# Optimization experiments

Hardware: AMD Instinct MI355X
Metric: run time of the kernel (lower is better)

## Reference

```python
import jax, jax.numpy as jnp
import numpy as np

B, H, K = 4096, 256, 16
INPUT_DIM, XPRIME_DIM = 8, 64
D = INPUT_DIM * XPRIME_DIM  # 512
LN_EPS = 1e-5


def setup_inputs() -> dict:
    key = jax.random.key(0)
    ks = jax.random.split(key, 12)
    s1 = 1.0  # Linear(1, D): fan_in=1
    sD = 1.0 / np.sqrt(D)
    sH = 1.0 / np.sqrt(H)
    return {
        "h_prev_rnn": jax.random.normal(ks[0], (B, H), jnp.float32),
        "x_l": jax.random.normal(ks[1], (B, INPUT_DIM), jnp.float32),
        "x_ext": jax.random.normal(ks[2], (B, K), jnp.float32),
        # stacked per-expert MetaNet params
        "meta_w1": jax.random.uniform(ks[3], (K, D), jnp.float32, -s1, s1),
        "meta_b1": jax.random.uniform(ks[4], (K, D), jnp.float32, -s1, s1),
        "meta_w2": jax.random.uniform(ks[5], (K, D, D), jnp.float32, -sD, sD),
        "meta_b2": jax.random.uniform(ks[6], (K, D), jnp.float32, -sD, sD),
        # gating net
        "gw1": jax.random.uniform(ks[7], (H, H), jnp.float32, -sH, sH),
        "gb1": jax.random.uniform(ks[8], (H,), jnp.float32, -sH, sH),
        "gw2": jax.random.uniform(ks[9], (H, K), jnp.float32, -sH, sH),
        "gb2": jax.random.uniform(ks[10], (K,), jnp.float32, -sH, sH),
        # LayerNorm([input_dim, xprime_dim]) affine params
        "ln_g": jnp.ones((INPUT_DIM, XPRIME_DIM), jnp.float32),
        "ln_b": jnp.zeros((INPUT_DIM, XPRIME_DIM), jnp.float32),
        "theta0": jnp.zeros((1, INPUT_DIM, XPRIME_DIM), jnp.float32),
    }


def reference(h_prev_rnn, x_l, x_ext, meta_w1, meta_b1, meta_w2, meta_b2,
              gw1, gb1, gw2, gb2, ln_g, ln_b, theta0):
    # MetaNet layer1 (Linear(1, D)): scalar input per expert -> [B, K, D]
    h1 = jnp.tanh(x_ext[:, :, None] * meta_w1[None] + meta_b1[None])
    # MetaNet layer2: per-expert DxD GEMM
    h2 = jnp.tanh(jnp.einsum('bkd,kde->bke', h1, meta_w2) + meta_b2[None])
    W = h2.reshape(h2.shape[0], K, INPUT_DIM, XPRIME_DIM)  # [B,K,i,e]
    # LayerNorm over last two dims jointly, affine
    mu = W.mean(axis=(-2, -1), keepdims=True)
    var = W.var(axis=(-2, -1), keepdims=True)
    W = (W - mu) * jax.lax.rsqrt(var + LN_EPS) * ln_g + ln_b
    # gating: softmax over experts (epoch/top_k = None path)
    logits = jnp.tanh(h_prev_rnn @ gw1 + gb1) @ gw2 + gb2
    gates = jax.nn.softmax(logits, axis=-1)  # [B, K]
    theta = jnp.einsum('bk,bkie->bie', gates, W) + theta0  # [B, i, e]
    x_prime = jnp.einsum('bi,bie->be', x_l, theta)  # [B, e]
    return (x_prime, theta)
```

## Files before the change

kernel.cpp:

```cpp
#include <hip/hip_runtime.h>
#include <stdint.h>

#define NB 4096
#define NH 256
#define NK 16
#define ND 512
#define NC 48
#define NM 48
#define RCHEB 7.0f
#define PI_F 3.14159265358979323846f
#define CCPART (NK * 2 * ND * 32)

typedef _Float16 f16;
using half8   = __attribute__((ext_vector_type(8))) _Float16;
using float4v = __attribute__((ext_vector_type(4))) float;

__device__ __forceinline__ float fast_tanh(float x) {
  float e = __builtin_amdgcn_exp2f(x * 2.88539008177793f);
  return 1.0f - 2.0f * __builtin_amdgcn_rcpf(e + 1.0f);
}

template <int CTRL>
__device__ __forceinline__ float dpp_addstep(float x) {
  int y = __builtin_amdgcn_update_dpp(0, __builtin_bit_cast(int, x),
                                      CTRL, 0xf, 0xf, true);
  return x + __builtin_bit_cast(float, y);
}
__device__ __forceinline__ float rowsum16(float x) {
  x = dpp_addstep<0xB1>(x);
  x = dpp_addstep<0x4E>(x);
  x = dpp_addstep<0x141>(x);
  x = dpp_addstep<0x140>(x);
  return x;
}

__global__ __launch_bounds__(256) void k_gs(
    const float* __restrict__ h_prev,
    const float* __restrict__ gw1, const float* __restrict__ gb1,
    const float* __restrict__ gw2, const float* __restrict__ gb2,
    const float* __restrict__ w1, const float* __restrict__ b1,
    float* __restrict__ gates, float* __restrict__ Sg, float* __restrict__ ctg) {
  __shared__ float sbuf[4096];
  const int t = threadIdx.x;
  const int blk = blockIdx.x;

  if (blk >= 512) {
    const int sb = blk - 512;
    const int k = sb >> 3;
    const int d0 = (sb & 7) * 64;
    if (sb == 0) {
      for (int i = t; i < NM * NC; i += 256) {
        const int m = i / 48, j = i - m * 48;
        const int r = (j * (2 * m + 1)) % 192;
        const float fac = (j == 0 ? 1.0f : 2.0f) * (1.0f / 48.0f);
        ctg[i] = cosf(PI_F * (float)r * (1.0f / 96.0f)) * fac;
      }
    }
    const int dl = t >> 2, mg = t & 3;
    const int d = d0 + dl;
    const float a = w1[k * ND + d];
    const float b = b1[k * ND + d];
    float o[12];
#pragma unroll
    for (int mi = 0; mi < 12; ++mi) {
      const int m = mg * 12 + mi;
      const float cx = cosf(PI_F * (float)(2 * m + 1) * (1.0f / 96.0f));
      o[mi] = fast_tanh(fmaf(a, RCHEB * cx, b));
    }
    float* dst = Sg + ((size_t)k * ND + d) * NM + mg * 12;
    *(float4*)&dst[0] = *(float4*)&o[0];
    *(float4*)&dst[4] = *(float4*)&o[4];
    *(float4*)&dst[8] = *(float4*)&o[8];
    return;
  }

  const int b0 = blk * 8;
  float* sh_h = sbuf;
  float* sh_t = sbuf + 2048;
  for (int r = 0; r < 8; ++r) sh_h[r * 256 + t] = h_prev[(b0 + r) * NH + t];
  __syncthreads();
  float acc[8];
  const float bias = gb1[t];
#pragma unroll
  for (int r = 0; r < 8; ++r) acc[r] = bias;
  for (int i = 0; i < NH; i += 4) {
    const float w0 = gw1[(i + 0) * NH + t];
    const float w1v = gw1[(i + 1) * NH + t];
    const float w2v = gw1[(i + 2) * NH + t];
    const float w3 = gw1[(i + 3) * NH + t];
#pragma unroll
    for (int r = 0; r < 8; ++r) {
      const float4 hv = *(const float4*)&sh_h[r * 256 + i];
      acc[r] += hv.x * w0 + hv.y * w1v + hv.z * w2v + hv.w * w3;
    }
  }
#pragma unroll
  for (int r = 0; r < 8; ++r) sh_t[t * 8 + r] = fast_tanh(acc[r]);
  __syncthreads();
  if (t < 128) {
    const int r = t >> 4, k = t & 15;
    float lg = gb2[k];
    for (int j = 0; j < NH; ++j) lg += sh_t[j * 8 + r] * gw2[j * NK + k];
    float m = lg;
    for (int off = 1; off < 16; off <<= 1) m = fmaxf(m, __shfl_xor(m, off, 16));
    const float e = __builtin_amdgcn_exp2f((lg - m) * 1.44269504f);
    float s = e;
    for (int off = 1; off < 16; off <<= 1) s += __shfl_xor(s, off, 16);
    gates[(b0 + r) * NK + k] = e * __builtin_amdgcn_rcpf(s);
  }
}

__global__ __launch_bounds__(256) void k_coef(
    const float* __restrict__ w2, const float* __restrict__ Sg,
    const float* __restrict__ ctg, float* __restrict__ Cc) {
  __shared__ float Gl[48][68];
  const int t = threadIdx.x;
  const int blk = blockIdx.x;
  const int k = blk >> 5;
  const int e0 = ((blk >> 2) & 7) * 64;
  const int dq = blk & 3;
  const int el = t & 63;
  const int mqu = __builtin_amdgcn_readfirstlane(t >> 6);

  const float* w2p = w2 + ((size_t)k * ND + dq * 128) * ND + e0 + el;
  const float* Sp = Sg + ((size_t)k * ND + dq * 128) * NM + mqu * 12;

  float g[12];
#pragma unroll
  for (int i = 0; i < 12; ++i) g[i] = 0.f;
#pragma unroll 4
  for (int d = 0; d < 128; ++d) {
    const float wv = w2p[(size_t)d * ND];
    const float4 s0 = *(const float4*)&Sp[d * NM];
    const float4 s1 = *(const float4*)&Sp[d * NM + 4];
    const float4 s2 = *(const float4*)&Sp[d * NM + 8];
    g[0] = fmaf(s0.x, wv, g[0]);
    g[1] = fmaf(s0.y, wv, g[1]);
    g[2] = fmaf(s0.z, wv, g[2]);
    g[3] = fmaf(s0.w, wv, g[3]);
    g[4] = fmaf(s1.x, wv, g[4]);
    g[5] = fmaf(s1.y, wv, g[5]);
    g[6] = fmaf(s1.z, wv, g[6]);
    g[7] = fmaf(s1.w, wv, g[7]);
    g[8] = fmaf(s2.x, wv, g[8]);
    g[9] = fmaf(s2.y, wv, g[9]);
    g[10] = fmaf(s2.z, wv, g[10]);
    g[11] = fmaf(s2.w, wv, g[11]);
  }

#pragma unroll
  for (int mi = 0; mi < 12; ++mi) Gl[mqu * 12 + mi][el] = g[mi];
  __syncthreads();

  float cacc[12];
#pragma unroll
  for (int i = 0; i < 12; ++i) cacc[i] = 0.f;
#pragma unroll 4
  for (int m = 0; m < NM; ++m) {
    const float gv = Gl[m][el];
    const float4 c0 = *(const float4*)&ctg[m * 48 + mqu * 12];
    const float4 c1 = *(const float4*)&ctg[m * 48 + mqu * 12 + 4];
    const float4 c2 = *(const float4*)&ctg[m * 48 + mqu * 12 + 8];
    cacc[0] = fmaf(c0.x, gv, cacc[0]);
    cacc[1] = fmaf(c0.y, gv, cacc[1]);
    cacc[2] = fmaf(c0.z, gv, cacc[2]);
    cacc[3] = fmaf(c0.w, gv, cacc[3]);
    cacc[4] = fmaf(c1.x, gv, cacc[4]);
    cacc[5] = fmaf(c1.y, gv, cacc[5]);
    cacc[6] = fmaf(c1.z, gv, cacc[6]);
    cacc[7] = fmaf(c1.w, gv, cacc[7]);
    cacc[8] = fmaf(c2.x, gv, cacc[8]);
    cacc[9] = fmaf(c2.y, gv, cacc[9]);
    cacc[10] = fmaf(c2.z, gv, cacc[10]);
    cacc[11] = fmaf(c2.w, gv, cacc[11]);
  }
  float* Ccq = Cc + (size_t)dq * CCPART;
#pragma unroll
  for (int jj = 0; jj < 12; ++jj) {
    const int j = mqu * 12 + jj;
    Ccq[((size_t)(k * 2 + (j >> 5)) * ND + e0 + el) * 32 + (j & 31)] = cacc[jj];
  }
}

__global__ __launch_bounds__(256) void k_pack(
    const float* __restrict__ Cc, const float* __restrict__ b2,
    f16* __restrict__ Cbf) {
  const int idx = blockIdx.x * 256 + threadIdx.x;
  const int flat8 = idx * 8;
  const int k2 = flat8 >> 14;
  const int rem = flat8 & 16383;
  const int e = rem >> 5, o8 = rem & 31;
  const int j0 = (k2 & 1) * 32 + o8;
  f16 o[8];
  if (j0 >= 48) {
#pragma unroll
    for (int i = 0; i < 8; ++i) o[i] = (f16)0.f;
  } else {
    float v[8];
#pragma unroll
    for (int i = 0; i < 8; ++i) v[i] = 0.f;
#pragma unroll
    for (int p = 0; p < 4; ++p) {
      const float4 u0 = *(const float4*)&Cc[(size_t)p * CCPART + flat8];
      const float4 u1 = *(const float4*)&Cc[(size_t)p * CCPART + flat8 + 4];
      v[0] += u0.x; v[1] += u0.y; v[2] += u0.z; v[3] += u0.w;
      v[4] += u1.x; v[5] += u1.y; v[6] += u1.z; v[7] += u1.w;
    }
    if (((k2 & 1) == 0) && (o8 == 0)) v[0] += b2[(k2 >> 1) * ND + e];
#pragma unroll
    for (int i = 0; i < 8; ++i) o[i] = (f16)v[i];
  }
  *(uint4*)&Cbf[flat8] = *(uint4*)o;
}

__global__ __launch_bounds__(512) void k_eval(
    const f16* __restrict__ Cbf, const float* __restrict__ gates,
    const float* __restrict__ x_ext, const float* __restrict__ x_l,
    const float* __restrict__ ln_g, const float* __restrict__ ln_b,
    const float* __restrict__ theta0, float* __restrict__ out) {
  __shared__ __align__(16) char sm[55808];
  f16* Tlds = (f16*)sm;
  float (*xp)[16][68] = (float(*)[16][68])sm;
  float (*lnbuf)[16][8][2] = (float(*)[16][8][2])(sm + 36864);
  float (*sx)[16] = (float(*)[16])(sm + 53248);
  float (*sg)[16] = (float(*)[16])(sm + 54272);
  float (*sxl)[8] = (float(*)[8])(sm + 55296);
  const int t = threadIdx.x;
  const int l = t & 63, wn = t >> 6;
  const int q = l >> 4, m16 = l & 15;
  const int b0 = blockIdx.x * 16;

  const f16* Bbase = Cbf + ((size_t)(wn * 64 + m16)) * 32 + q * 8;
  half8 BrA[8], BrB[8];
  auto loadB = [&](int k, half8(&dst)[8]) {
#pragma unroll
    for (int bni = 0; bni < 4; ++bni) {
      dst[bni * 2 + 0] =
          *(const half8*)(Bbase + ((size_t)(k * 2 + 0) * ND + bni * 16) * 32);
      dst[bni * 2 + 1] =
          *(const half8*)(Bbase + ((size_t)(k * 2 + 1) * ND + bni * 16) * 32);
    }
  };
  loadB(0, BrA);

  if (t < 256) {
    sx[t >> 4][t & 15] = x_ext[(b0 + (t >> 4)) * NK + (t & 15)];
    sg[t >> 4][t & 15] = gates[(b0 + (t >> 4)) * NK + (t & 15)];
  } else if (t < 384) {
    const int tt = t - 256;
    sxl[tt >> 3][tt & 7] = x_l[(b0 + (tt >> 3)) * 8 + (tt & 7)];
  }
  __syncthreads();

  if (t < 256) {
    const int k = t >> 4, row = t & 15;
    f16* T0 = &Tlds[(2 * k) * 576 + row * 36];
    f16* T1 = &Tlds[(2 * k + 1) * 576 + row * 36];
    float u = sx[row][k] * (1.0f / RCHEB);
    u = fminf(1.0f, fmaxf(-1.0f, u));
    const float u2 = u + u;
    float tp = 1.0f, tc = u;
    T0[0] = (f16)1.0f;
    T0[1] = (f16)u;
#pragma unroll
    for (int j = 2; j < 48; ++j) {
      const float tn = fmaf(u2, tc, -tp);
      tp = tc; tc = tn;
      if (j < 32) T0[j] = (f16)tn; else T1[j - 32] = (f16)tn;
    }
#pragma unroll
    for (int j = 48; j < 64; ++j) T1[j - 32] = (f16)0.f;
  }
  __syncthreads();

  float lng[4], lnb[4];
#pragma unroll
  for (int bni = 0; bni < 4; ++bni) {
    const int col = wn * 64 + bni * 16 + m16;
    lng[bni] = ln_g[col];
    lnb[bni] = ln_b[col];
  }

  float th[4][4];
#pragma unroll
  for (int bni = 0; bni < 4; ++bni)
#pragma unroll
    for (int rr = 0; rr < 4; ++rr) th[bni][rr] = 0.f;

  const f16* Abase = Tlds + m16 * 36 + q * 8;
  const float4v z = {0.f, 0.f, 0.f, 0.f};

  auto stepA = [&](int k, const half8(&Br)[8], float4v(&acc)[4],
                   float(&s)[4], float(&s2)[4]) {
    const half8 a0 = *(const half8*)(Abase + (2 * k) * 576);
    const half8 a1 = *(const half8*)(Abase + (2 * k + 1) * 576);
#pragma unroll
    for (int bni = 0; bni < 4; ++bni) {
      acc[bni] = __builtin_amdgcn_mfma_f32_16x16x32_f16(a0, Br[2 * bni], z, 0, 0, 0);
      acc[bni] = __builtin_amdgcn_mfma_f32_16x16x32_f16(a1, Br[2 * bni + 1],
                                                        acc[bni], 0, 0, 0);
    }
#pragma unroll
    for (int rr = 0; rr < 4; ++rr) { s[rr] = 0.f; s2[rr] = 0.f; }
#pragma unroll
    for (int bni = 0; bni < 4; ++bni)
#pragma unroll
      for (int rr = 0; rr < 4; ++rr) {
        const float v = fast_tanh(acc[bni][rr]);
        acc[bni][rr] = v;
        s[rr] += v;
        s2[rr] = fmaf(v, v, s2[rr]);
      }
#pragma unroll
    for (int rr = 0; rr < 4; ++rr) {
      s[rr] = rowsum16(s[rr]);
      s2[rr] = rowsum16(s2[rr]);
    }
  };
  auto lnwrite = [&](int k, const float(&s)[4], const float(&s2)[4]) {
    if (m16 == 0) {
#pragma unroll
      for (int rr = 0; rr < 4; ++rr)
        *(float2*)&lnbuf[k][q * 4 + rr][wn][0] = make_float2(s[rr], s2[rr]);
    }
  };
  auto apply = [&](int k, const float4v(&acc)[4]) {
#pragma unroll
    for (int rr = 0; rr < 4; ++rr) {
      const int row = q * 4 + rr;
      const float4 pa = *(const float4*)&lnbuf[k][row][0][0];
      const float4 pb = *(const float4*)&lnbuf[k][row][2][0];
      const float4 pc = *(const float4*)&lnbuf[k][row][4][0];
      const float4 pd = *(const float4*)&lnbuf[k][row][6][0];
      const float S1 = pa.x + pa.z + pb.x + pb.z + pc.x + pc.z + pd.x + pd.z;
      const float S2 = pa.y + pa.w + pb.y + pb.w + pc.y + pc.w + pd.y + pd.w;
      const float mu = S1 * (1.0f / 512.0f);
      const float var = fmaf(S2, 1.0f / 512.0f, -mu * mu);
      const float rs = __builtin_amdgcn_rsqf(var + 1e-5f);
      const float gate = sg[row][k];
      const float a = gate * rs;
#pragma unroll
      for (int bni = 0; bni < 4; ++bni)
        th[bni][rr] = fmaf(a * lng[bni], acc[bni][rr] - mu,
                           fmaf(gate, lnb[bni], th[bni][rr]));
    }
  };

  float sA[4], s2A[4], sB[4], s2B[4];
  float4v accA[4], accB[4];

  stepA(0, BrA, accA, sA, s2A);
  lnwrite(0, sA, s2A);
  loadB(1, BrB);
  __syncthreads();
  for (int kp = 0; kp < 7; ++kp) {
    stepA(2 * kp + 1, BrB, accB, sB, s2B);
    apply(2 * kp, accA);
    lnwrite(2 * kp + 1, sB, s2B);
    loadB(2 * kp + 2, BrA);
    __syncthreads();
    stepA(2 * kp + 2, BrA, accA, sA, s2A);
    apply(2 * kp + 1, accB);
    lnwrite(2 * kp + 2, sA, s2A);
    loadB(2 * kp + 3, BrB);
    __syncthreads();
  }
  stepA(15, BrB, accB, sB, s2B);
  apply(14, accA);
  lnwrite(15, sB, s2B);
  __syncthreads();
  apply(15, accB);

  float* thbase = out + (size_t)NB * 64;
#pragma unroll
  for (int bni = 0; bni < 4; ++bni) {
    const int col = wn * 64 + bni * 16 + m16;
    const float t0v = theta0[col];
#pragma unroll
    for (int rr = 0; rr < 4; ++rr) {
      const float o = th[bni][rr] + t0v;
      th[bni][rr] = o;
      thbase[(size_t)(b0 + q * 4 + rr) * ND + col] = o;
    }
  }
#pragma unroll
  for (int rr = 0; rr < 4; ++rr) {
    const int row = q * 4 + rr;
    const float xlw = sxl[row][wn];
#pragma unroll
    for (int bni = 0; bni < 4; ++bni)
      xp[wn][row][bni * 16 + m16] = xlw * th[bni][rr];
  }
  __syncthreads();
  {
    const int idx = t * 2;
    const int row = idx >> 6, ec = idx & 63;
    float2 r = {0.f, 0.f};
#pragma unroll
    for (int w8 = 0; w8 < 8; ++w8) {
      const float2 p = *(const float2*)&xp[w8][row][ec];
      r.x += p.x;
      r.y += p.y;
    }
    *(float2*)&out[(size_t)(b0 + row) * 64 + ec] = r;
  }
}

extern "C" void kernel_launch(void* const* d_in, const int* in_sizes, int n_in,
                              void* d_out, int out_size, void* d_ws, size_t ws_size,
                              hipStream_t stream) {
  const float* h_prev = (const float*)d_in[0];
  const float* x_l    = (const float*)d_in[1];
  const float* x_ext  = (const float*)d_in[2];
  const float* mw1    = (const float*)d_in[3];
  const float* mb1    = (const float*)d_in[4];
  const float* mw2    = (const float*)d_in[5];
  const float* mb2    = (const float*)d_in[6];
  const float* gw1    = (const float*)d_in[7];
  const float* gb1    = (const float*)d_in[8];
  const float* gw2    = (const float*)d_in[9];
  const float* gb2    = (const float*)d_in[10];
  const float* ln_g   = (const float*)d_in[11];
  const float* ln_b   = (const float*)d_in[12];
  const float* th0    = (const float*)d_in[13];
  float* out = (float*)d_out;

  char* ws = (char*)d_ws;
  float* gates = (float*)ws;
  f16* Cbf     = (f16*)(ws + 0x40000);
  float* Cc    = (float*)(ws + 0x140000);
  float* Sg    = (float*)(ws + 0x940000);
  float* ctg   = (float*)(ws + 0xB00000);

  hipLaunchKernelGGL(k_gs, dim3(640), dim3(256), 0, stream,
                     h_prev, gw1, gb1, gw2, gb2, mw1, mb1, gates, Sg, ctg);
  hipLaunchKernelGGL(k_coef, dim3(512), dim3(256), 0, stream,
                     mw2, Sg, ctg, Cc);
  hipLaunchKernelGGL(k_pack, dim3(256), dim3(256), 0, stream,
                     Cc, mb2, Cbf);
  hipLaunchKernelGGL(k_eval, dim3(256), dim3(512), 0, stream,
                     Cbf, gates, x_ext, x_l, ln_g, ln_b, th0, out);
}
```

Baseline: 166.9 us.

## Shrink eval LDS and registers with single-buffered LN stats and transposed gating weights

In the eval kernel, the per-expert LayerNorm statistics buffer becomes a single slot. One wave computes per-row scale, shift and gate scalars, and the other waves read them back. The double-buffered accumulators are dropped, cutting LDS and register use so more blocks can be resident. The price is two barriers per expert step instead of one, and the MFMA work no longer overlaps the normalization. Separately, the gating kernel transposes gw2 into LDS and vectorizes the second-layer dot product.

```diff
diff --git a/kernel.cpp b/kernel.cpp
--- a/kernel.cpp
+++ b/kernel.cpp
@@ -40,7 +40,7 @@
     const float* __restrict__ gw2, const float* __restrict__ gb2,
     const float* __restrict__ w1, const float* __restrict__ b1,
     float* __restrict__ gates, float* __restrict__ Sg, float* __restrict__ ctg) {
-  __shared__ float sbuf[4096];
+  __shared__ __align__(16) float sbuf[8288];
   const int t = threadIdx.x;
   const int blk = blockIdx.x;
 
@@ -74,10 +74,18 @@
     return;
   }
 
-  const int b0 = blk * 8;
   float* sh_h = sbuf;
   float* sh_t = sbuf + 2048;
+  float* gw2t = sbuf + 4128;
+  const int b0 = blk * 8;
   for (int r = 0; r < 8; ++r) sh_h[r * 256 + t] = h_prev[(b0 + r) * NH + t];
+  {
+    float4 gr[4];
+#pragma unroll
+    for (int i4 = 0; i4 < 4; ++i4) gr[i4] = *(const float4*)&gw2[t * NK + i4 * 4];
+#pragma unroll
+    for (int kk = 0; kk < 16; ++kk) gw2t[kk * 260 + t] = ((const float*)gr)[kk];
+  }
   __syncthreads();
   float acc[8];
   const float bias = gb1[t];
@@ -95,12 +103,17 @@
     }
   }
 #pragma unroll
-  for (int r = 0; r < 8; ++r) sh_t[t * 8 + r] = fast_tanh(acc[r]);
+  for (int r = 0; r < 8; ++r) sh_t[r * 260 + t] = fast_tanh(acc[r]);
   __syncthreads();
   if (t < 128) {
     const int r = t >> 4, k = t & 15;
     float lg = gb2[k];
-    for (int j = 0; j < NH; ++j) lg += sh_t[j * 8 + r] * gw2[j * NK + k];
+#pragma unroll 8
+    for (int j4 = 0; j4 < 64; ++j4) {
+      const float4 tv = *(const float4*)&sh_t[r * 260 + j4 * 4];
+      const float4 wv = *(const float4*)&gw2t[k * 260 + j4 * 4];
+      lg += tv.x * wv.x + tv.y * wv.y + tv.z * wv.z + tv.w * wv.w;
+    }
     float m = lg;
     for (int off = 1; off < 16; off <<= 1) m = fmaxf(m, __shfl_xor(m, off, 16));
     const float e = __builtin_amdgcn_exp2f((lg - m) * 1.44269504f);
@@ -218,13 +231,14 @@
     const float* __restrict__ x_ext, const float* __restrict__ x_l,
     const float* __restrict__ ln_g, const float* __restrict__ ln_b,
     const float* __restrict__ theta0, float* __restrict__ out) {
-  __shared__ __align__(16) char sm[55808];
+  __shared__ __align__(16) char sm[40960];
   f16* Tlds = (f16*)sm;
   float (*xp)[16][68] = (float(*)[16][68])sm;
-  float (*lnbuf)[16][8][2] = (float(*)[16][8][2])(sm + 36864);
-  float (*sx)[16] = (float(*)[16])(sm + 53248);
-  float (*sg)[16] = (float(*)[16])(sm + 54272);
-  float (*sxl)[8] = (float(*)[8])(sm + 55296);
+  float* lnbuf = (float*)(sm + 36864);
+  float* scal  = (float*)(sm + 38144);
+  float (*sx)[16] = (float(*)[16])(sm + 38400);
+  float (*sg)[16] = (float(*)[16])(sm + 39424);
+  float (*sxl)[8] = (float(*)[8])(sm + 40448);
   const int t = threadIdx.x;
   const int l = t & 63, wn = t >> 6;
   const int q = l >> 4, m16 = l & 15;
@@ -290,8 +304,10 @@
   const f16* Abase = Tlds + m16 * 36 + q * 8;
   const float4v z = {0.f, 0.f, 0.f, 0.f};
 
-  auto stepA = [&](int k, const half8(&Br)[8], float4v(&acc)[4],
-                   float(&s)[4], float(&s2)[4]) {
+  float4v acc[4];
+  float s[4], s2[4];
+
+  auto stepA = [&](int k, const half8(&Br)[8]) {
     const half8 a0 = *(const half8*)(Abase + (2 * k) * 576);
     const half8 a1 = *(const half8*)(Abase + (2 * k + 1) * 576);
 #pragma unroll
@@ -316,60 +332,57 @@
       s[rr] = rowsum16(s[rr]);
       s2[rr] = rowsum16(s2[rr]);
     }
+    if (m16 == 0) {
+#pragma unroll
+      for (int rr = 0; rr < 4; ++rr)
+        *(float2*)&lnbuf[(q * 4 + rr) * 20 + wn * 2] = make_float2(s[rr], s2[rr]);
+    }
   };
-  auto lnwrite = [&](int k, const float(&s)[4], const float(&s2)[4]) {
-    if (m16 == 0) {
-#pragma unroll
-      for (int rr = 0; rr < 4; ++rr)
-        *(float2*)&lnbuf[k][q * 4 + rr][wn][0] = make_float2(s[rr], s2[rr]);
-    }
-  };
-  auto apply = [&](int k, const float4v(&acc)[4]) {
-#pragma unroll
-    for (int rr = 0; rr < 4; ++rr) {
-      const int row = q * 4 + rr;
-      const float4 pa = *(const float4*)&lnbuf[k][row][0][0];
-      const float4 pb = *(const float4*)&lnbuf[k][row][2][0];
-      const float4 pc = *(const float4*)&lnbuf[k][row][4][0];
-      const float4 pd = *(const float4*)&lnbuf[k][row][6][0];
-      const float S1 = pa.x + pa.z + pb.x + pb.z + pc.x + pc.z + pd.x + pd.z;
-      const float S2 = pa.y + pa.w + pb.y + pb.w + pc.y + pc.w + pd.y + pd.w;
+  auto scalc = [&](int k) {
+    if (wn == 0 && l < 16) {
+      const int row = l;
+      const float4 p0 = *(const float4*)&lnbuf[row * 20 + 0];
+      const float4 p1 = *(const float4*)&lnbuf[row * 20 + 4];
+      const float4 p2 = *(const float4*)&lnbuf[row * 20 + 8];
+      const float4 p3 = *(const float4*)&lnbuf[row * 20 + 12];
+      const float S1 = p0.x + p0.z + p1.x + p1.z + p2.x + p2.z + p3.x + p3.z;
+      const float S2 = p0.y + p0.w + p1.y + p1.w + p2.y + p2.w + p3.y + p3.w;
       const float mu = S1 * (1.0f / 512.0f);
       const float var = fmaf(S2, 1.0f / 512.0f, -mu * mu);
       const float rs = __builtin_amdgcn_rsqf(var + 1e-5f);
       const float gate = sg[row][k];
-      const float a = gate * rs;
+      const float A = gate * rs;
+      *(float4*)&scal[row * 4] = make_float4(A, A * mu, gate, 0.0f);
+    }
+  };
+  auto apply = [&]() {
+#pragma unroll
+    for (int rr = 0; rr < 4; ++rr) {
+      const int row = q * 4 + rr;
+      const float4 sc = *(const float4*)&scal[row * 4];
+      const float A = sc.x, M = sc.y, gate = sc.z;
 #pragma unroll
       for (int bni = 0; bni < 4; ++bni)
-        th[bni][rr] = fmaf(a * lng[bni], acc[bni][rr] - mu,
-                           fmaf(gate, lnb[bni], th[bni][rr]));
+        th[bni][rr] = fmaf(A * lng[bni], acc[bni][rr],
+                       fmaf(-M, lng[bni],
+                        fmaf(gate, lnb[bni], th[bni][rr])));
     }
   };
 
-  float sA[4], s2A[4], sB[4], s2B[4];
-  float4v accA[4], accB[4];
-
-  stepA(0, BrA, accA, sA, s2A);
-  lnwrite(0, sA, s2A);
-  loadB(1, BrB);
-  __syncthreads();
-  for (int kp = 0; kp < 7; ++kp) {
-    stepA(2 * kp + 1, BrB, accB, sB, s2B);
-    apply(2 * kp, accA);
-    lnwrite(2 * kp + 1, sB, s2B);
-    loadB(2 * kp + 2, BrA);
+  for (int kp = 0; kp < 8; ++kp) {
+    stepA(2 * kp, BrA);
+    loadB(2 * kp + 1, BrB);
     __syncthreads();
-    stepA(2 * kp + 2, BrA, accA, sA, s2A);
-    apply(2 * kp + 1, accB);
-    lnwrite(2 * kp + 2, sA, s2A);
-    loadB(2 * kp + 3, BrB);
+    scalc(2 * kp);
     __syncthreads();
-  }
-  stepA(15, BrB, accB, sB, s2B);
-  apply(14, accA);
-  lnwrite(15, sB, s2B);
-  __syncthreads();
-  apply(15, accB);
+    apply();
+    stepA(2 * kp + 1, BrB);
+    if (kp < 7) loadB(2 * kp + 2, BrA);
+    __syncthreads();
+    scalc(2 * kp + 1);
+    __syncthreads();
+    apply();
+  }
 
   float* thbase = out + (size_t)NB * 64;
 #pragma unroll
@@ -383,6 +396,7 @@
       thbase[(size_t)(b0 + q * 4 + rr) * ND + col] = o;
     }
   }
+  __syncthreads();
 #pragma unroll
   for (int rr = 0; rr < 4; ++rr) {
     const int row = q * 4 + rr;
```

New measurement: 161.7 us. 3.1% less time.
